# Kernel optimization log

Measured on AMD Instinct MI355X. Metric: run time of the kernel, lower is better.

## Reference

```python
import jax, jax.numpy as jnp
import numpy as np

N, E, F, H = 20000, 320000, 128, 256   # nodes, edges, in-features, hidden
M, NQ = 4096, 2048                      # lsq rows, QP variables
LAMB_MAX = 2.0


def setup_inputs() -> dict:
    key = jax.random.key(0)
    ks = jax.random.split(key, 12)
    x = jax.random.normal(ks[0], (N, F), jnp.float32)
    edge_index = jax.random.randint(ks[1], (2, E), 0, N)
    A = jax.random.normal(ks[2], (M, NQ), jnp.float32) * 0.05
    b = jax.random.normal(ks[3], (M, 1), jnp.float32)
    feat_ids = jax.random.randint(ks[4], (NQ,), 0, N)
    x_prior = jax.random.uniform(ks[5], (NQ, 1), jnp.float32)
    lamb = jnp.ones((1,), jnp.float32)
    # ChebConv K=2 weights: one linear per Chebyshev order, plus bias
    W10 = jax.random.normal(ks[6], (F, H), jnp.float32) / np.sqrt(F)
    W11 = jax.random.normal(ks[7], (F, H), jnp.float32) / np.sqrt(F)
    b1 = jnp.zeros((H,), jnp.float32)
    W20 = jax.random.normal(ks[8], (H, 1), jnp.float32) / np.sqrt(H)
    W21 = jax.random.normal(ks[9], (H, 1), jnp.float32) / np.sqrt(H)
    b2 = jnp.zeros((1,), jnp.float32)
    return {"x": x, "edge_index": edge_index, "A": A, "b": b,
            "feat_ids": feat_ids, "x_prior": x_prior, "lamb": lamb,
            "W10": W10, "W11": W11, "b1": b1,
            "W20": W20, "W21": W21, "b2": b2}


def _cheb_conv(x, edge_index, W0, W1, bias, lam_max):
    """PyG ChebConv with K=2: out = x @ W0 + (2L/lam_max - I) x @ W1 + bias,
    L = I - D^{-1/2} A D^{-1/2}, via edge gather/scatter (no dense NxN)."""
    row, col = edge_index[0], edge_index[1]
    n = x.shape[0]
    deg = jax.ops.segment_sum(jnp.ones_like(row, dtype=x.dtype), row, num_segments=n)
    dinv = jnp.where(deg > 0, deg ** -0.5, 0.0)
    # normalized edge weight scaled by 2/lam_max, negated (off-diag of L_hat)
    w = -(2.0 / lam_max) * dinv[row] * dinv[col]              # [E]
    msg = jax.ops.segment_sum(w[:, None] * x[col], row, num_segments=n)
    Tx1 = msg + (2.0 / lam_max - 1.0) * x                      # diagonal of L_hat
    return x @ W0 + Tx1 @ W1 + bias


def reference(x, edge_index, A, b, feat_ids, x_prior, lamb,
              W10, W11, b1, W20, W21, b2):
    h = jax.nn.relu(_cheb_conv(x, edge_index, W10, W11, b1, LAMB_MAX))
    h = lamb[0] * jax.nn.relu(_cheb_conv(h, edge_index, W20, W21, b2, LAMB_MAX))
    hfold = h[feat_ids] + 1e-5                                 # [NQ, 1]
    q = hfold[:, 0]
    # QP: min 1/2 z^T Q z + p^T z with vacuous inequality (0*z <= 0.1) and no
    # equality constraints -> interior-point converges to unconstrained min.
    Q = A.T @ A + jnp.diag(q)                                  # [NQ, NQ]
    p = -(x_prior * hfold)[:, 0] - (b.T @ A)[0]                # [NQ]
    z = jnp.linalg.solve(Q, -p)                                # [NQ]
    return z[:, None]                                          # f.T -> [NQ, 1]
```

## Files before the change

### kernel.cpp

```cpp
#include <hip/hip_runtime.h>

#define N_NODES 20000
#define N_EDGES 320000
#define F_DIM   128
#define H_DIM   256
#define M_ROWS  4096
#define NQ      2048
#define NIT     18
#define MM_ROWS 20032

typedef __attribute__((ext_vector_type(8))) short short8;
typedef __attribute__((ext_vector_type(4))) float f32x4;


__device__ __forceinline__ float wred(float v) {
#pragma unroll
  for (int m = 32; m > 0; m >>= 1) v += __shfl_xor(v, m, 64);
  return v;
}

__device__ __forceinline__ float bred256(float v, float* lds) {
  v = wred(v);
  int w = threadIdx.x >> 6;
  if ((threadIdx.x & 63) == 0) lds[w] = v;
  __syncthreads();
  float tot = lds[0] + lds[1] + lds[2] + lds[3];
  __syncthreads();
  return tot;
}

__device__ __forceinline__ unsigned f2bf(float f) {
  unsigned u = __float_as_uint(f);
  unsigned r = u + 0x7fffu + ((u >> 16) & 1u);
  return r >> 16;
}
__device__ __forceinline__ float bflo(unsigned u) { return __uint_as_float(u << 16); }
__device__ __forceinline__ float bfhi(unsigned u) { return __uint_as_float(u & 0xffff0000u); }


__global__ __launch_bounds__(256) void k_deg(const int* __restrict__ ei, int* __restrict__ deg) {
  int e = blockIdx.x * 256 + threadIdx.x;
  if (e < N_EDGES) atomicAdd(&deg[ei[e]], 1);
}

__global__ __launch_bounds__(1024) void k_scan(const int* __restrict__ deg,
    int* __restrict__ rowstart, float* __restrict__ dinv) {
  __shared__ int part[1024];
  int t = threadIdx.x;
  const int chunk = (N_NODES + 1023) / 1024;
  int lo = t * chunk;
  int hi = lo + chunk; if (hi > N_NODES) hi = N_NODES;
  int s = 0;
  for (int i = lo; i < hi; ++i) {
    int d = deg[i];
    dinv[i] = d > 0 ? rsqrtf((float)d) : 0.f;
    s += d;
  }
  part[t] = s;
  __syncthreads();
  for (int off = 1; off < 1024; off <<= 1) {
    int v = part[t];
    int add = (t >= off) ? part[t - off] : 0;
    __syncthreads();
    part[t] = v + add;
    __syncthreads();
  }
  int base = (t > 0) ? part[t - 1] : 0;
  for (int i = lo; i < hi; ++i) { rowstart[i] = base; base += deg[i]; }
  if (t == 0) rowstart[N_NODES] = part[1023];
}

__global__ __launch_bounds__(256) void k_scatter(const int* __restrict__ ei,
    const int* __restrict__ rowstart, int* __restrict__ cursor,
    const float* __restrict__ dinv, int* __restrict__ cols, float* __restrict__ wvals) {
  int e = blockIdx.x * 256 + threadIdx.x;
  if (e >= N_EDGES) return;
  int r = ei[e];
  int c = ei[N_EDGES + e];
  int pos = rowstart[r] + atomicAdd(&cursor[r], 1);
  cols[pos] = c;
  wvals[pos] = -dinv[r] * dinv[c];
}

#define CONVX_BLKS (MM_ROWS * 16 / 256)

__global__ __launch_bounds__(256) void k_pack(const float* __restrict__ x,
    const float* __restrict__ W10, const float* __restrict__ W11,
    unsigned* __restrict__ xu, unsigned* __restrict__ Wtb) {
  int bx = blockIdx.x;
  if (bx < CONVX_BLKS) {
    int gid = bx * 256 + threadIdx.x;
    int row = gid >> 4;
    int q8 = gid & 15;
    uint4* xu4 = (uint4*)xu;
    if (row < N_NODES) {
      const float4* x4 = (const float4*)x;
      float4 a = x4[(size_t)row * 32 + q8 * 2];
      float4 b = x4[(size_t)row * 32 + q8 * 2 + 1];
      uint4 u;
      u.x = f2bf(a.x) | (f2bf(a.y) << 16);
      u.y = f2bf(a.z) | (f2bf(a.w) << 16);
      u.z = f2bf(b.x) | (f2bf(b.y) << 16);
      u.w = f2bf(b.z) | (f2bf(b.w) << 16);
      xu4[(size_t)row * 32 + q8] = u;
    } else {
      uint4 z = make_uint4(0, 0, 0, 0);
      xu4[(size_t)row * 32 + q8] = z;
      xu4[(size_t)row * 32 + 16 + q8] = z;
    }
  } else {
    int gid = (bx - CONVX_BLKS) * 256 + threadIdx.x;
    int n = gid >> 7;
    int u = gid & 127;
    int k0 = u * 2;
    float v0 = (k0 < 128) ? W10[(size_t)k0 * H_DIM + n]
                          : W11[(size_t)(k0 - 128) * H_DIM + n];
    float v1 = (k0 + 1 < 128) ? W10[(size_t)(k0 + 1) * H_DIM + n]
                              : W11[(size_t)(k0 - 127) * H_DIM + n];
    Wtb[(size_t)n * 128 + u] = f2bf(v0) | (f2bf(v1) << 16);
  }
}

__global__ __launch_bounds__(256) void k_msg1(const int* __restrict__ rowstart,
    const int* __restrict__ cols, const float* __restrict__ wvals,
    unsigned* __restrict__ xu) {
  int wid = (blockIdx.x * 256 + threadIdx.x) >> 6;
  int lane = threadIdx.x & 63;
  if (wid >= N_NODES) return;
  int s0 = rowstart[wid], s1 = rowstart[wid + 1];
  float2 acc = make_float2(0.f, 0.f);
  for (int e = s0; e < s1; ++e) {
    int c = cols[e];
    float w = wvals[e];
    unsigned u = xu[(size_t)c * 128 + lane];
    acc.x += w * bflo(u);
    acc.y += w * bfhi(u);
  }
  xu[(size_t)wid * 128 + 64 + lane] = f2bf(acc.x) | (f2bf(acc.y) << 16);
}


__device__ __forceinline__ void mm_ldfrag(short8* Af, short8* Bf,
    const unsigned* __restrict__ xurow, const unsigned* __restrict__ wrow, int kc) {
#pragma unroll
  for (int a = 0; a < 4; ++a)
    Af[a] = *(const short8*)(xurow + (size_t)a * 16 * 128 + kc * 16);
#pragma unroll
  for (int n = 0; n < 4; ++n)
    Bf[n] = *(const short8*)(wrow + (size_t)n * 16 * 128 + kc * 16);
}

__global__ __launch_bounds__(256) void k_mm(const unsigned* __restrict__ xu,
    const unsigned* __restrict__ Wtb, const float* __restrict__ b1,
    const float* __restrict__ W20, const float* __restrict__ W21,
    float* __restrict__ t, float* __restrict__ s) {
  const int row0 = blockIdx.x * 64;
  const int tid = threadIdx.x;
  const int w = tid >> 6, lane = tid & 63;
  const int colb = w * 64;
  const int frow = lane & 15, fqo = (lane >> 4) * 4;
  const int c16 = lane & 15, q4 = lane >> 4;

  f32x4 acc[4][4];
#pragma unroll
  for (int a = 0; a < 4; ++a)
#pragma unroll
    for (int b = 0; b < 4; ++b) {
      acc[a][b][0] = 0.f; acc[a][b][1] = 0.f;
      acc[a][b][2] = 0.f; acc[a][b][3] = 0.f;
    }

  const unsigned* xurow = xu + (size_t)(row0 + frow) * 128 + fqo;
  const unsigned* wrow  = Wtb + (size_t)(colb + frow) * 128 + fqo;

  short8 A0[4], B0[4], A1[4], B1[4];
  mm_ldfrag(A0, B0, xurow, wrow, 0);
#pragma unroll
  for (int kp = 0; kp < 4; ++kp) {
    const int kc = kp * 2;
    mm_ldfrag(A1, B1, xurow, wrow, kc + 1);
#pragma unroll
    for (int a = 0; a < 4; ++a)
#pragma unroll
      for (int n = 0; n < 4; ++n)
        acc[a][n] = __builtin_amdgcn_mfma_f32_16x16x32_bf16(A0[a], B0[n], acc[a][n], 0, 0, 0);
    if (kc + 2 < 8) mm_ldfrag(A0, B0, xurow, wrow, kc + 2);
#pragma unroll
    for (int a = 0; a < 4; ++a)
#pragma unroll
      for (int n = 0; n < 4; ++n)
        acc[a][n] = __builtin_amdgcn_mfma_f32_16x16x32_bf16(A1[a], B1[n], acc[a][n], 0, 0, 0);
  }

  float tp[4][4] = {}, sp[4][4] = {};
#pragma unroll
  for (int b2 = 0; b2 < 4; ++b2) {
    int gc = colb + b2 * 16 + c16;
    float w20 = W20[gc], w21 = W21[gc], bb = b1[gc];
#pragma unroll
    for (int a = 0; a < 4; ++a)
#pragma unroll
      for (int r = 0; r < 4; ++r) {
        float val = acc[a][b2][r] + bb;
        val = val > 0.f ? val : 0.f;
        tp[a][r] += val * w20;
        sp[a][r] += val * w21;
      }
  }
#pragma unroll
  for (int a = 0; a < 4; ++a)
#pragma unroll
    for (int r = 0; r < 4; ++r) {
#pragma unroll
      for (int m = 1; m < 16; m <<= 1) {
        tp[a][r] += __shfl_xor(tp[a][r], m, 64);
        sp[a][r] += __shfl_xor(sp[a][r], m, 64);
      }
    }
  if (c16 == 0) {
#pragma unroll
    for (int a = 0; a < 4; ++a)
#pragma unroll
      for (int r = 0; r < 4; ++r) {
        int gr = row0 + a * 16 + q4 * 4 + r;
        if (gr < N_NODES) {
          atomicAdd(&t[gr], tp[a][r]);
          atomicAdd(&s[gr], sp[a][r]);
        }
      }
  }
}


__global__ __launch_bounds__(256) void k_h2(const float* __restrict__ t,
    const float* __restrict__ s, const int* __restrict__ rowstart,
    const int* __restrict__ cols, const float* __restrict__ wvals,
    const float* __restrict__ lamb, const float* __restrict__ b2, float* __restrict__ h2) {
  int i = blockIdx.x * 256 + threadIdx.x;
  if (i >= N_NODES) return;
  float m = 0.f;
  int s0 = rowstart[i], s1 = rowstart[i + 1];
  for (int e = s0; e < s1; ++e) m += wvals[e] * s[cols[e]];
  float val = t[i] + m + b2[0];
  val = val > 0.f ? val : 0.f;
  h2[i] = lamb[0] * val;
}

__global__ __launch_bounds__(256) void k_prep(const float* __restrict__ A,
    const float* __restrict__ b, unsigned* __restrict__ Atu, float* __restrict__ btA_parts) {
  int jp = blockIdx.x * 256 + threadIdx.x;
  int k0 = blockIdx.y * 128;
  const float2* A2 = (const float2*)A;
  float acc0 = 0.f, acc1 = 0.f;
  for (int kk = 0; kk < 128; kk += 8) {
    float ax[8], ay[8];
#pragma unroll
    for (int i = 0; i < 8; ++i) {
      int k = k0 + kk + i;
      float2 a = A2[(size_t)k * 1024 + jp];
      float bk = b[k];
      acc0 += a.x * bk;
      acc1 += a.y * bk;
      ax[i] = a.x; ay[i] = a.y;
    }
    uint4 t0, t1;
    t0.x = f2bf(ax[0]) | (f2bf(ax[1]) << 16);
    t0.y = f2bf(ax[2]) | (f2bf(ax[3]) << 16);
    t0.z = f2bf(ax[4]) | (f2bf(ax[5]) << 16);
    t0.w = f2bf(ax[6]) | (f2bf(ax[7]) << 16);
    t1.x = f2bf(ay[0]) | (f2bf(ay[1]) << 16);
    t1.y = f2bf(ay[2]) | (f2bf(ay[3]) << 16);
    t1.z = f2bf(ay[4]) | (f2bf(ay[5]) << 16);
    t1.w = f2bf(ay[6]) | (f2bf(ay[7]) << 16);
    int uoff = (k0 + kk) >> 1;
    *(uint4*)(Atu + (size_t)(2 * jp) * 2048 + uoff) = t0;
    *(uint4*)(Atu + (size_t)(2 * jp + 1) * 2048 + uoff) = t1;
  }
  ((float2*)(btA_parts + (size_t)blockIdx.y * NQ))[jp] = make_float2(acc0, acc1);
}

__global__ __launch_bounds__(256) void k_qrhs(const float* __restrict__ h2,
    const int* __restrict__ feat_ids, const float* __restrict__ x_prior,
    const float* __restrict__ btA_parts, float* __restrict__ q, float* __restrict__ r) {
  int j = blockIdx.x * 256 + threadIdx.x;
  int f = feat_ids[j];
  float hf = h2[f] + 1e-5f;
  q[j] = hf;
  float bta = 0.f;
#pragma unroll
  for (int c = 0; c < 32; ++c) bta += btA_parts[(size_t)c * NQ + j];
  r[j] = x_prior[j] * hf + bta;
}

#define GR_ST 20
#define NTILE 136

__global__ __launch_bounds__(512) void k_gram(const unsigned* __restrict__ Atu,
                                              float* __restrict__ Gp) {
  __shared__ unsigned shA[128 * GR_ST];
  __shared__ unsigned shB[128 * GR_ST];
  const int bid = blockIdx.x;
  const int wid = (bid & 7) * 68 + (bid >> 3);
  const int tile = wid >> 2;
  const int kq = wid & 3;
  int uu = tile, bi = 0;
  while (uu >= 16 - bi) { uu -= 16 - bi; ++bi; }
  const int bj = bi + uu;
  const int i0 = bi * 128, j0 = bj * 128;
  const int tid = threadIdx.x;
  const int w = tid >> 6, lane = tid & 63;
  const int wr = (w >> 2) * 64, wc = (w & 3) * 32;
  const int srow = tid >> 2, suo = (tid & 3) * 4;
  const int frow = lane & 15, fqo = (lane >> 4) * 4;

  f32x4 acc[4][2];
#pragma unroll
  for (int a = 0; a < 4; ++a)
#pragma unroll
    for (int b = 0; b < 2; ++b) {
      acc[a][b][0] = 0.f; acc[a][b][1] = 0.f;
      acc[a][b][2] = 0.f; acc[a][b][3] = 0.f;
    }

  const unsigned* pa = Atu + (size_t)(i0 + srow) * 2048 + kq * 512 + suo;
  const unsigned* pb = Atu + (size_t)(j0 + srow) * 2048 + kq * 512 + suo;

  uint4 ra = *(const uint4*)(pa);
  uint4 rb = *(const uint4*)(pb);

  unsigned* as = shA + srow * GR_ST + suo;
  unsigned* bs = shB + srow * GR_ST + suo;

  for (int si = 0; si < 32; ++si) {
    *(uint4*)as = ra;
    *(uint4*)bs = rb;
    if (si + 1 < 32) {
      const int ku = (si + 1) * 16;
      ra = *(const uint4*)(pa + ku);
      rb = *(const uint4*)(pb + ku);
    }
    __syncthreads();
    short8 af[4], bf[2];
#pragma unroll
    for (int a = 0; a < 4; ++a)
      af[a] = *(const short8*)(shA + (wr + a * 16 + frow) * GR_ST + fqo);
#pragma unroll
    for (int b2 = 0; b2 < 2; ++b2)
      bf[b2] = *(const short8*)(shB + (wc + b2 * 16 + frow) * GR_ST + fqo);
#pragma unroll
    for (int a = 0; a < 4; ++a)
#pragma unroll
      for (int b2 = 0; b2 < 2; ++b2)
        acc[a][b2] = __builtin_amdgcn_mfma_f32_16x16x32_bf16(af[a], bf[b2], acc[a][b2], 0, 0, 0);
    __syncthreads();
  }

  const int q4 = lane >> 4, c16 = lane & 15;
  float* Gz = Gp + ((size_t)kq * NTILE + tile) * 16384;
#pragma unroll
  for (int a = 0; a < 4; ++a)
#pragma unroll
    for (int b2 = 0; b2 < 2; ++b2)
#pragma unroll
      for (int r = 0; r < 4; ++r) {
        int lr = wr + a * 16 + q4 * 4 + r;
        int lc = wc + b2 * 16 + c16;
        Gz[lr * 128 + lc] = acc[a][b2][r];
      }
}

#define GT_ST 131

__global__ __launch_bounds__(256) void k_gconv(const float* __restrict__ Gp,
    const float* __restrict__ q, unsigned* __restrict__ Gb, float* __restrict__ qcorr) {
  __shared__ unsigned short T[128 * GT_ST];
  int uu = blockIdx.x, bi = 0;
  while (uu >= 16 - bi) { uu -= 16 - bi; ++bi; }
  const int bj = bi + uu;
  const int tid = threadIdx.x;
  const int r = tid >> 1, ch = (tid & 1) * 64;
  const size_t tile = (size_t)blockIdx.x * 16384;
  const float4* P0 = (const float4*)(Gp + tile + r * 128 + ch);
  const float4* P1 = (const float4*)(Gp + (size_t)1 * NTILE * 16384 + tile + r * 128 + ch);
  const float4* P2 = (const float4*)(Gp + (size_t)2 * NTILE * 16384 + tile + r * 128 + ch);
  const float4* P3 = (const float4*)(Gp + (size_t)3 * NTILE * 16384 + tile + r * 128 + ch);
  const int gr = bi * 128 + r;
  const bool hasdiag = (bi == bj) && (r >= ch) && (r < ch + 64);
  unsigned uo[32];
#pragma unroll
  for (int j = 0; j < 16; ++j) {
    float4 a = P0[j], b = P1[j], c = P2[j], d = P3[j];
    float v0 = a.x + b.x + c.x + d.x;
    float v1 = a.y + b.y + c.y + d.y;
    float v2 = a.z + b.z + c.z + d.z;
    float v3 = a.w + b.w + c.w + d.w;
    const int c0 = ch + j * 4;
    if (hasdiag && (r - c0 >= 0) && (r - c0 < 4)) {
      float qv = q[gr];
      int dsel = r - c0;
      if (dsel == 0) v0 += qv;
      else if (dsel == 1) v1 += qv;
      else if (dsel == 2) v2 += qv;
      else v3 += qv;
      float vd = (dsel == 0) ? v0 : (dsel == 1) ? v1 : (dsel == 2) ? v2 : v3;
      qcorr[gr] = vd - bflo(f2bf(vd));
    }
    unsigned u0 = f2bf(v0) | (f2bf(v1) << 16);
    unsigned u1 = f2bf(v2) | (f2bf(v3) << 16);
    uo[2 * j] = u0;
    uo[2 * j + 1] = u1;
    T[r * GT_ST + c0]     = (unsigned short)(u0 & 0xffffu);
    T[r * GT_ST + c0 + 1] = (unsigned short)(u0 >> 16);
    T[r * GT_ST + c0 + 2] = (unsigned short)(u1 & 0xffffu);
    T[r * GT_ST + c0 + 3] = (unsigned short)(u1 >> 16);
  }
  uint4* dst = (uint4*)(Gb + (size_t)gr * 1024 + bj * 64 + (ch >> 1));
#pragma unroll
  for (int j = 0; j < 8; ++j) dst[j] = ((const uint4*)uo)[j];
  __syncthreads();
  if (bi != bj) {
    const int wv = tid >> 6, lane = tid & 63;
    for (int kk = 0; kk < 32; ++kk) {
      int rr = kk * 4 + wv;
      unsigned lo = T[(2 * lane) * GT_ST + rr];
      unsigned hi = T[(2 * lane + 1) * GT_ST + rr];
      Gb[(size_t)(bj * 128 + rr) * 1024 + bi * 64 + lane] = lo | (hi << 16);
    }
  }
}

__global__ __launch_bounds__(256) void k_cgG(int k, const unsigned* __restrict__ Gb,
    const float* __restrict__ qcorr,
    const float* __restrict__ r_old, float* __restrict__ r_new,
    const float* __restrict__ p_old, float* __restrict__ p_new,
    const float* __restrict__ Qp_in, float* __restrict__ Qp_out,
    float* __restrict__ xcg) {
  __shared__ float pshare[NQ];
  __shared__ float lds[4];
  const int tid = threadIdx.x, bid = blockIdx.x;
  const float4* r4 = (const float4*)r_old;
  float4 ra = r4[tid * 2], rb2 = r4[tid * 2 + 1];
  float pv[8];
  if (k == 0) {
    pv[0] = ra.x; pv[1] = ra.y; pv[2] = ra.z; pv[3] = ra.w;
    pv[4] = rb2.x; pv[5] = rb2.y; pv[6] = rb2.z; pv[7] = rb2.w;
    if (bid == 0) {
      ((float4*)p_new)[tid * 2] = ra;
      ((float4*)p_new)[tid * 2 + 1] = rb2;
    }
  } else {
    const float4* p4 = (const float4*)p_old;
    const float4* qp4 = (const float4*)Qp_in;
    float4 pa = p4[tid * 2], pb = p4[tid * 2 + 1];
    float4 qa = qp4[tid * 2], qb = qp4[tid * 2 + 1];
    float rr = ra.x * ra.x + ra.y * ra.y + ra.z * ra.z + ra.w * ra.w +
               rb2.x * rb2.x + rb2.y * rb2.y + rb2.z * rb2.z + rb2.w * rb2.w;
    float pap = pa.x * qa.x + pa.y * qa.y + pa.z * qa.z + pa.w * qa.w +
                pb.x * qb.x + pb.y * qb.y + pb.z * qb.z + pb.w * qb.w;
    rr = bred256(rr, lds);
    pap = bred256(pap, lds);
    float alpha = rr / pap;
    if (bid == 0) {
      float4* x4 = (float4*)xcg;
      float4 xa = x4[tid * 2], xb = x4[tid * 2 + 1];
      xa.x += alpha * pa.x; xa.y += alpha * pa.y;
      xa.z += alpha * pa.z; xa.w += alpha * pa.w;
      xb.x += alpha * pb.x; xb.y += alpha * pb.y;
      xb.z += alpha * pb.z; xb.w += alpha * pb.w;
      x4[tid * 2] = xa; x4[tid * 2 + 1] = xb;
    }
    ra.x -= alpha * qa.x; ra.y -= alpha * qa.y;
    ra.z -= alpha * qa.z; ra.w -= alpha * qa.w;
    rb2.x -= alpha * qb.x; rb2.y -= alpha * qb.y;
    rb2.z -= alpha * qb.z; rb2.w -= alpha * qb.w;
    float rrn = ra.x * ra.x + ra.y * ra.y + ra.z * ra.z + ra.w * ra.w +
                rb2.x * rb2.x + rb2.y * rb2.y + rb2.z * rb2.z + rb2.w * rb2.w;
    rrn = bred256(rrn, lds);
    float beta = rrn / rr;
    pv[0] = ra.x + beta * pa.x; pv[1] = ra.y + beta * pa.y;
    pv[2] = ra.z + beta * pa.z; pv[3] = ra.w + beta * pa.w;
    pv[4] = rb2.x + beta * pb.x; pv[5] = rb2.y + beta * pb.y;
    pv[6] = rb2.z + beta * pb.z; pv[7] = rb2.w + beta * pb.w;
    if (bid == 0) {
      ((float4*)r_new)[tid * 2] = ra;
      ((float4*)r_new)[tid * 2 + 1] = rb2;
      ((float4*)p_new)[tid * 2] = make_float4(pv[0], pv[1], pv[2], pv[3]);
      ((float4*)p_new)[tid * 2 + 1] = make_float4(pv[4], pv[5], pv[6], pv[7]);
    }
  }
  ((float4*)pshare)[tid * 2] = make_float4(pv[0], pv[1], pv[2], pv[3]);
  ((float4*)pshare)[tid * 2 + 1] = make_float4(pv[4], pv[5], pv[6], pv[7]);
  __syncthreads();
  const int w = tid >> 6, lane = tid & 63;
  const int row0 = bid * 8 + w * 2;
  const uint4* Gr0 = (const uint4*)(Gb + (size_t)row0 * 1024);
  const uint4* Gr1 = (const uint4*)(Gb + (size_t)(row0 + 1) * 1024);
  const float4* ps4 = (const float4*)pshare;
  float acc0 = 0.f, acc1 = 0.f;
#pragma unroll
  for (int c = 0; c < 4; ++c) {
    uint4 g0 = Gr0[c * 64 + lane];
    uint4 g1 = Gr1[c * 64 + lane];
    float4 pa = ps4[c * 128 + lane * 2];
    float4 pb = ps4[c * 128 + lane * 2 + 1];
    acc0 += bflo(g0.x) * pa.x + bfhi(g0.x) * pa.y;
    acc0 += bflo(g0.y) * pa.z + bfhi(g0.y) * pa.w;
    acc0 += bflo(g0.z) * pb.x + bfhi(g0.z) * pb.y;
    acc0 += bflo(g0.w) * pb.z + bfhi(g0.w) * pb.w;
    acc1 += bflo(g1.x) * pa.x + bfhi(g1.x) * pa.y;
    acc1 += bflo(g1.y) * pa.z + bfhi(g1.y) * pa.w;
    acc1 += bflo(g1.z) * pb.x + bfhi(g1.z) * pb.y;
    acc1 += bflo(g1.w) * pb.z + bfhi(g1.w) * pb.w;
  }
  acc0 = wred(acc0);
  acc1 = wred(acc1);
  if (lane == 0) {
    Qp_out[row0] = acc0 + qcorr[row0] * pshare[row0];
    Qp_out[row0 + 1] = acc1 + qcorr[row0 + 1] * pshare[row0 + 1];
  }
}

__global__ __launch_bounds__(256) void k_cgfin(const float* __restrict__ r_last,
    const float* __restrict__ p_last, const float* __restrict__ Qp,
    const float* __restrict__ xcg, float* __restrict__ out) {
  const int tid = threadIdx.x;
  const int lane = tid & 63;
  const float4* r4 = (const float4*)r_last;
  const float4* p4 = (const float4*)p_last;
  const float4* q4 = (const float4*)Qp;
  float rr = 0.f, pap = 0.f;
#pragma unroll
  for (int c = 0; c < 4; ++c) {
#pragma unroll
    for (int hh = 0; hh < 2; ++hh) {
      float4 rv = r4[c * 128 + lane * 2 + hh];
      float4 pv = p4[c * 128 + lane * 2 + hh];
      float4 qv = q4[c * 128 + lane * 2 + hh];
      rr += rv.x * rv.x + rv.y * rv.y + rv.z * rv.z + rv.w * rv.w;
      pap += pv.x * qv.x + pv.y * qv.y + pv.z * qv.z + pv.w * qv.w;
    }
  }
  rr = wred(rr);
  pap = wred(pap);
  float alpha = rr / pap;
  const float4* x4 = (const float4*)xcg;
  float4* o4 = (float4*)out;
#pragma unroll
  for (int hh = 0; hh < 2; ++hh) {
    int i4 = tid * 2 + hh;
    float4 xv = x4[i4];
    float4 pv = p4[i4];
    xv.x += alpha * pv.x; xv.y += alpha * pv.y;
    xv.z += alpha * pv.z; xv.w += alpha * pv.w;
    o4[i4] = xv;
  }
}


extern "C" void kernel_launch(void* const* d_in, const int* in_sizes, int n_in,
                              void* d_out, int out_size, void* d_ws, size_t ws_size,
                              hipStream_t stream) {
  const float* x      = (const float*)d_in[0];
  const int*   ei     = (const int*)d_in[1];
  const float* A      = (const float*)d_in[2];
  const float* b      = (const float*)d_in[3];
  const int*   fids   = (const int*)d_in[4];
  const float* xprior = (const float*)d_in[5];
  const float* lamb   = (const float*)d_in[6];
  const float* W10    = (const float*)d_in[7];
  const float* W11    = (const float*)d_in[8];
  const float* b1     = (const float*)d_in[9];
  const float* W20    = (const float*)d_in[10];
  const float* W21    = (const float*)d_in[11];
  const float* b2     = (const float*)d_in[12];
  float* out = (float*)d_out;

  char* base = (char*)d_ws;
  size_t o = 0;
  auto alloc = [&](size_t bytes) { size_t r = o; o = (o + bytes + 255) & ~size_t(255); return r; };

  size_t off_deg    = alloc(N_NODES * 4);
  size_t off_cursor = alloc(N_NODES * 4);
  size_t off_xcg    = alloc(NQ * 4);
  size_t off_t      = alloc(N_NODES * 4);
  size_t off_s      = alloc(N_NODES * 4);
  size_t zero_end   = o;
  size_t off_rowst  = alloc((N_NODES + 1) * 4);
  size_t off_dinv   = alloc(N_NODES * 4);
  size_t off_h2     = alloc(N_NODES * 4);
  size_t off_q      = alloc(NQ * 4);
  size_t off_r0     = alloc(NQ * 4);
  size_t off_r1     = alloc(NQ * 4);
  size_t off_p0     = alloc(NQ * 4);
  size_t off_p1     = alloc(NQ * 4);
  size_t off_Qp0    = alloc(NQ * 4);
  size_t off_Qp1    = alloc(NQ * 4);
  size_t off_qcorr  = alloc(NQ * 4);
  size_t off_btAp   = alloc(32 * NQ * 4);
  size_t off_Wtb    = alloc(256 * 128 * 4);
  size_t sz_cols  = (size_t)N_EDGES * 4 + 256;
  size_t sz_wvals = (size_t)N_EDGES * 4 + 256;
  size_t sz_xmsg  = (size_t)MM_ROWS * 256 * 2;
  size_t union_gnn = sz_cols + sz_wvals + sz_xmsg;
  size_t union_at  = (size_t)M_ROWS * NQ * 2;
  size_t off_union = alloc(union_gnn > union_at ? union_gnn : union_at);
  size_t off_Gp    = alloc((size_t)4 * NTILE * 16384 * 4);
  if (o > ws_size) return;

  int*   deg      = (int*)(base + off_deg);
  int*   cursor   = (int*)(base + off_cursor);
  float* xcg      = (float*)(base + off_xcg);
  float* t        = (float*)(base + off_t);
  float* s        = (float*)(base + off_s);
  int*   rowstart = (int*)(base + off_rowst);
  float* dinv     = (float*)(base + off_dinv);
  float* h2       = (float*)(base + off_h2);
  float* q        = (float*)(base + off_q);
  float* rb[2]    = {(float*)(base + off_r0), (float*)(base + off_r1)};
  float* pg[2]    = {(float*)(base + off_p0), (float*)(base + off_p1)};
  float* Qpb[2]   = {(float*)(base + off_Qp0), (float*)(base + off_Qp1)};
  float* qcorr    = (float*)(base + off_qcorr);
  float* btA_parts = (float*)(base + off_btAp);
  unsigned* Wtb   = (unsigned*)(base + off_Wtb);
  int*   cols     = (int*)(base + off_union);
  float* wvals    = (float*)(base + off_union + sz_cols);
  unsigned* xmsgb = (unsigned*)(base + off_union + sz_cols + sz_wvals);
  unsigned* Atu   = (unsigned*)(base + off_union);
  unsigned* Gb    = (unsigned*)(base + off_union);
  float* Gp       = (float*)(base + off_Gp);

  hipMemsetAsync(d_ws, 0, zero_end, stream);

  k_deg<<<(N_EDGES + 255) / 256, 256, 0, stream>>>(ei, deg);
  k_scan<<<1, 1024, 0, stream>>>(deg, rowstart, dinv);
  k_scatter<<<(N_EDGES + 255) / 256, 256, 0, stream>>>(ei, rowstart, cursor, dinv, cols, wvals);

  k_pack<<<CONVX_BLKS + 128, 256, 0, stream>>>(x, W10, W11, xmsgb, Wtb);
  k_msg1<<<N_NODES / 4, 256, 0, stream>>>(rowstart, cols, wvals, xmsgb);
  k_mm<<<MM_ROWS / 64, 256, 0, stream>>>(xmsgb, Wtb, b1, W20, W21, t, s);
  k_h2<<<(N_NODES + 255) / 256, 256, 0, stream>>>(t, s, rowstart, cols, wvals, lamb, b2, h2);

  k_prep<<<dim3(4, 32), 256, 0, stream>>>(A, b, Atu, btA_parts);
  k_qrhs<<<NQ / 256, 256, 0, stream>>>(h2, fids, xprior, btA_parts, q, rb[0]);
  k_gram<<<544, 512, 0, stream>>>(Atu, Gp);
  k_gconv<<<NTILE, 256, 0, stream>>>(Gp, q, Gb, qcorr);

  k_cgG<<<256, 256, 0, stream>>>(0, Gb, qcorr, rb[0], rb[0], pg[0], pg[0],
                                 Qpb[1], Qpb[0], xcg);
  for (int k = 1; k < NIT; ++k) {
    k_cgG<<<256, 256, 0, stream>>>(k, Gb, qcorr, rb[(k - 1) & 1], rb[k & 1],
                                   pg[(k - 1) & 1], pg[k & 1],
                                   Qpb[(k - 1) & 1], Qpb[k & 1], xcg);
  }
  k_cgfin<<<1, 256, 0, stream>>>(rb[(NIT - 1) & 1], pg[(NIT - 1) & 1],
                                 Qpb[(NIT - 1) & 1], xcg, out);
}
```

Before: 400.5 us.

## Load Gram MFMA fragments directly from global memory with register double-buffering

The Gram-matrix kernel stops staging A^T tiles through shared memory. Each wave now loads its bf16 MFMA fragments straight from global memory into registers and double-buffers them across k-steps, which removes both __syncthreads per step. Blocks shrink from 512 to 256 threads, and each wave computes a 64x64 sub-tile instead of 64x32. This raises per-wave register use and drops the sharing of loads across waves through LDS, so global and L2 traffic for fragments goes up. It also relies on the cache to absorb the strided, row-wise fragment loads.

New measurement: 453.0 us. 1.13x slower.

```diff
diff --git a/kernel.cpp b/kernel.cpp
--- a/kernel.cpp
+++ b/kernel.cpp
@@ -292,13 +292,20 @@
   r[j] = x_prior[j] * hf + bta;
 }
 
-#define GR_ST 20
 #define NTILE 136
 
-__global__ __launch_bounds__(512) void k_gram(const unsigned* __restrict__ Atu,
+__device__ __forceinline__ void gr_ldfrag(short8* Af, short8* Bf,
+    const unsigned* __restrict__ pa, const unsigned* __restrict__ pb, int si) {
+#pragma unroll
+  for (int a = 0; a < 4; ++a)
+    Af[a] = *(const short8*)(pa + (size_t)a * 16 * 2048 + si * 16);
+#pragma unroll
+  for (int b = 0; b < 4; ++b)
+    Bf[b] = *(const short8*)(pb + (size_t)b * 16 * 2048 + si * 16);
+}
+
+__global__ __launch_bounds__(256) void k_gram(const unsigned* __restrict__ Atu,
                                               float* __restrict__ Gp) {
-  __shared__ unsigned shA[128 * GR_ST];
-  __shared__ unsigned shB[128 * GR_ST];
   const int bid = blockIdx.x;
   const int wid = (bid & 7) * 68 + (bid >> 3);
   const int tile = wid >> 2;
@@ -306,53 +313,39 @@
   int uu = tile, bi = 0;
   while (uu >= 16 - bi) { uu -= 16 - bi; ++bi; }
   const int bj = bi + uu;
-  const int i0 = bi * 128, j0 = bj * 128;
   const int tid = threadIdx.x;
   const int w = tid >> 6, lane = tid & 63;
-  const int wr = (w >> 2) * 64, wc = (w & 3) * 32;
-  const int srow = tid >> 2, suo = (tid & 3) * 4;
+  const int wr = (w >> 1) * 64, wc = (w & 1) * 64;
   const int frow = lane & 15, fqo = (lane >> 4) * 4;
 
-  f32x4 acc[4][2];
+  f32x4 acc[4][4];
 #pragma unroll
   for (int a = 0; a < 4; ++a)
 #pragma unroll
-    for (int b = 0; b < 2; ++b) {
+    for (int b = 0; b < 4; ++b) {
       acc[a][b][0] = 0.f; acc[a][b][1] = 0.f;
       acc[a][b][2] = 0.f; acc[a][b][3] = 0.f;
     }
 
-  const unsigned* pa = Atu + (size_t)(i0 + srow) * 2048 + kq * 512 + suo;
-  const unsigned* pb = Atu + (size_t)(j0 + srow) * 2048 + kq * 512 + suo;
-
-  uint4 ra = *(const uint4*)(pa);
-  uint4 rb = *(const uint4*)(pb);
-
-  unsigned* as = shA + srow * GR_ST + suo;
-  unsigned* bs = shB + srow * GR_ST + suo;
-
-  for (int si = 0; si < 32; ++si) {
-    *(uint4*)as = ra;
-    *(uint4*)bs = rb;
-    if (si + 1 < 32) {
-      const int ku = (si + 1) * 16;
-      ra = *(const uint4*)(pa + ku);
-      rb = *(const uint4*)(pb + ku);
-    }
-    __syncthreads();
-    short8 af[4], bf[2];
+  const unsigned* pa = Atu + (size_t)(bi * 128 + wr + frow) * 2048 + kq * 512 + fqo;
+  const unsigned* pb = Atu + (size_t)(bj * 128 + wc + frow) * 2048 + kq * 512 + fqo;
+
+  short8 A0[4], B0[4], A1[4], B1[4];
+  gr_ldfrag(A0, B0, pa, pb, 0);
+#pragma unroll
+  for (int sp = 0; sp < 16; ++sp) {
+    gr_ldfrag(A1, B1, pa, pb, 2 * sp + 1);
 #pragma unroll
     for (int a = 0; a < 4; ++a)
-      af[a] = *(const short8*)(shA + (wr + a * 16 + frow) * GR_ST + fqo);
-#pragma unroll
-    for (int b2 = 0; b2 < 2; ++b2)
-      bf[b2] = *(const short8*)(shB + (wc + b2 * 16 + frow) * GR_ST + fqo);
+#pragma unroll
+      for (int b2 = 0; b2 < 4; ++b2)
+        acc[a][b2] = __builtin_amdgcn_mfma_f32_16x16x32_bf16(A0[a], B0[b2], acc[a][b2], 0, 0, 0);
+    if (sp + 1 < 16) gr_ldfrag(A0, B0, pa, pb, 2 * sp + 2);
 #pragma unroll
     for (int a = 0; a < 4; ++a)
 #pragma unroll
-      for (int b2 = 0; b2 < 2; ++b2)
-        acc[a][b2] = __builtin_amdgcn_mfma_f32_16x16x32_bf16(af[a], bf[b2], acc[a][b2], 0, 0, 0);
-    __syncthreads();
+      for (int b2 = 0; b2 < 4; ++b2)
+        acc[a][b2] = __builtin_amdgcn_mfma_f32_16x16x32_bf16(A1[a], B1[b2], acc[a][b2], 0, 0, 0);
   }
 
   const int q4 = lane >> 4, c16 = lane & 15;
@@ -360,7 +353,7 @@
 #pragma unroll
   for (int a = 0; a < 4; ++a)
 #pragma unroll
-    for (int b2 = 0; b2 < 2; ++b2)
+    for (int b2 = 0; b2 < 4; ++b2)
 #pragma unroll
       for (int r = 0; r < 4; ++r) {
         int lr = wr + a * 16 + q4 * 4 + r;
@@ -642,7 +635,7 @@
 
   k_prep<<<dim3(4, 32), 256, 0, stream>>>(A, b, Atu, btA_parts);
   k_qrhs<<<NQ / 256, 256, 0, stream>>>(h2, fids, xprior, btA_parts, q, rb[0]);
-  k_gram<<<544, 512, 0, stream>>>(Atu, Gp);
+  k_gram<<<544, 256, 0, stream>>>(Atu, Gp);
   k_gconv<<<NTILE, 256, 0, stream>>>(Gp, q, Gb, qcorr);
 
   k_cgG<<<256, 256, 0, stream>>>(0, Gb, qcorr, rb[0], rb[0], pg[0], pg[0],
```
